# Kernel tuning notes

Hardware: AMD Instinct MI355X
Metric: run time of the kernel (lower is better)

## Reference

```python
import jax, jax.numpy as jnp
import numpy as np

TOP_K = 2


def setup_inputs() -> dict:
    key = jax.random.key(0)
    k_x, k_g, k_w1, k_w2, k_w3 = jax.random.split(key, 5)
    B, S, D, H, E = 2, 512, 1024, 512, 8
    x = jax.random.normal(k_x, (B, S, D), dtype=jnp.float32)
    gate_w = jax.random.normal(k_g, (D, E), dtype=jnp.float32) * (D ** -0.5)
    w1 = jax.random.normal(k_w1, (E, D, H), dtype=jnp.float32) * 0.02  # gate proj
    w2 = jax.random.normal(k_w2, (E, H, D), dtype=jnp.float32) * 0.02  # down proj
    w3 = jax.random.normal(k_w3, (E, D, H), dtype=jnp.float32) * 0.02  # up proj
    return {"x": x, "gate_w": gate_w, "w1": w1, "w2": w2, "w3": w3}


def reference(x, gate_w, w1, w2, w3):
    # Token-choice top-k MoE with grouped SwiGLU experts, no shared expert.
    # Equivalent to torchtune MoE: gather routed tokens, scale by top-k router
    # score, run per-expert FFN, scatter-add back. Since each expert's FFN has
    # no bias (FFN(0) == 0), the dispatch/grouped-GEMM/combine is expressed
    # densely as sum_e FFN_e(scale[:, e] * x), which is mathematically identical.
    B, S, D = x.shape
    E = gate_w.shape[1]
    xf = x.reshape(B * S, D)                      # [T, D]
    T = B * S

    logits = xf @ gate_w                          # [T, E]
    scores = jax.nn.softmax(logits, axis=-1)
    top_scores, top_idx = jax.lax.top_k(scores, TOP_K)  # [T, k]

    # scale[t, e] = router score if expert e selected for token t, else 0
    scale = jnp.zeros((T, E), dtype=x.dtype).at[
        jnp.arange(T)[:, None], top_idx
    ].set(top_scores)

    xs = scale.T[:, :, None] * xf[None, :, :]     # [E, T, D] scaled routed input
    h = jax.nn.silu(jnp.einsum('etd,edh->eth', xs, w1)) \
        * jnp.einsum('etd,edh->eth', xs, w3)      # [E, T, H]
    y = jnp.einsum('eth,ehd->etd', h, w2)         # [E, T, D]
    out = y.sum(axis=0)                           # combine (scatter-add equiv)
    return out.reshape(B, S, D)
```

## Files before the change

kernel.cpp:

```cpp
#include <hip/hip_runtime.h>
#include <hip/hip_bf16.h>
#include <cstddef>

#define T_TOK 1024
#define D_DIM 1024
#define H_DIM 512
#define E_EXP 8
#define P_CAP 2560
#define MAX_MT 72
#define LDA 72
#define NK1 16
#define NK2 8

typedef __attribute__((ext_vector_type(4))) float    float4_t;
typedef __attribute__((ext_vector_type(8))) short    short8_t;
typedef __attribute__((ext_vector_type(4))) unsigned uint4_t;
typedef __attribute__((ext_vector_type(2))) unsigned uint2_t;

__device__ __forceinline__ short f2bf(float f) {
  union { float f; unsigned u; } v; v.f = f;
  unsigned u = v.u;
  u += 0x7FFFu + ((u >> 16) & 1u);
  return (short)(u >> 16);
}

__device__ __forceinline__ unsigned pkbf(float a, float b) {
  union { __hip_bfloat162 h; unsigned u; } v;
  v.h = __float22bfloat162_rn(make_float2(a, b));
  return v.u;
}

__global__ __launch_bounds__(256) void prep_kernel(
    const float* __restrict__ w1, const float* __restrict__ w3,
    const float* __restrict__ w2, const float* __restrict__ x,
    const float* __restrict__ gw, short* __restrict__ w13t,
    short* __restrict__ w2t, int* __restrict__ idx2,
    float* __restrict__ scale2, float* __restrict__ out) {
  __shared__ float tile[64][69];
  const int z = blockIdx.z;
  const int tid = threadIdx.x;

  if (z < 24) {
    const float* src; short* dst; int N, ldd, row_off;
    if (z < 16) {
      if (blockIdx.y >= 8) return;
      int which = z >> 3, e = z & 7;
      src = (which ? w3 : w1) + (size_t)e * D_DIM * H_DIM;
      dst = w13t + (size_t)e * D_DIM * (2 * H_DIM);
      N = H_DIM; ldd = D_DIM; row_off = which ? H_DIM : 0;
    } else {
      if (blockIdx.x >= 8) return;
      int e = z - 16;
      src = w2 + (size_t)e * H_DIM * D_DIM;
      dst = w2t + (size_t)e * D_DIM * H_DIM;
      N = D_DIM; ldd = H_DIM; row_off = 0;
    }
    const int k0 = blockIdx.x * 64, n0 = blockIdx.y * 64;
    const int kr = tid >> 4, nc = (tid & 15) * 4;
    #pragma unroll
    for (int p = 0; p < 4; ++p) {
      int k = p * 16 + kr;
      float4_t v = *(const float4_t*)(src + (size_t)(k0 + k) * N + n0 + nc);
      tile[k][nc]     = v[0];
      tile[k][nc + 1] = v[1];
      tile[k][nc + 2] = v[2];
      tile[k][nc + 3] = v[3];
    }
    __syncthreads();
    const int r8 = tid >> 3, c8 = tid & 7;
    #pragma unroll
    for (int p = 0; p < 2; ++p) {
      int row = p * 32 + r8;
      uint4_t u;
      #pragma unroll
      for (int jj = 0; jj < 4; ++jj)
        u[jj] = pkbf(tile[c8 * 8 + 2 * jj][row], tile[c8 * 8 + 2 * jj + 1][row]);
      *(uint4_t*)(dst + (size_t)(row_off + n0 + row) * ldd + k0 + c8 * 8) = u;
    }
    return;
  }

  if (z == 25) {
    float4_t z4 = {0.f, 0.f, 0.f, 0.f};
    float4_t* o = (float4_t*)(out + ((size_t)(blockIdx.y * 16 + blockIdx.x)) * 4096);
    #pragma unroll
    for (int i = 0; i < 4; ++i) o[i * 256 + tid] = z4;
    return;
  }

  const int wid  = tid >> 6;
  const int lane = tid & 63;
  const int t = (blockIdx.y * 16 + blockIdx.x) * 4 + wid;
  const float* xr = x + (size_t)t * D_DIM;
  float acc[E_EXP];
  #pragma unroll
  for (int e = 0; e < E_EXP; ++e) acc[e] = 0.f;
  for (int d = lane; d < D_DIM; d += 64) {
    float xv = xr[d];
    float4_t g0 = *(const float4_t*)(gw + d * E_EXP);
    float4_t g1 = *(const float4_t*)(gw + d * E_EXP + 4);
    acc[0] += xv * g0[0]; acc[1] += xv * g0[1];
    acc[2] += xv * g0[2]; acc[3] += xv * g0[3];
    acc[4] += xv * g1[0]; acc[5] += xv * g1[1];
    acc[6] += xv * g1[2]; acc[7] += xv * g1[3];
  }
  #pragma unroll
  for (int off = 32; off >= 1; off >>= 1) {
    #pragma unroll
    for (int e = 0; e < E_EXP; ++e) acc[e] += __shfl_down(acc[e], off, 64);
  }
  if (lane == 0) {
    float m = acc[0];
    #pragma unroll
    for (int e = 1; e < E_EXP; ++e) m = fmaxf(m, acc[e]);
    float p[E_EXP]; float s = 0.f;
    #pragma unroll
    for (int e = 0; e < E_EXP; ++e) { p[e] = __expf(acc[e] - m); s += p[e]; }
    float inv = 1.f / s;
    #pragma unroll
    for (int e = 0; e < E_EXP; ++e) p[e] *= inv;
    int i1 = 0;
    #pragma unroll
    for (int e = 1; e < E_EXP; ++e) if (p[e] > p[i1]) i1 = e;
    int i2 = (i1 == 0) ? 1 : 0;
    #pragma unroll
    for (int e = 0; e < E_EXP; ++e) {
      if (e == i1 || e == i2) continue;
      if (p[e] > p[i2]) i2 = e;
    }
    idx2[2 * t]     = i1;  scale2[2 * t]     = p[i1];
    idx2[2 * t + 1] = i2;  scale2[2 * t + 1] = p[i2];
  }
}

__global__ __launch_bounds__(256) void scan_kernel(
    const int* __restrict__ idx2, const float* __restrict__ scale2,
    int* __restrict__ pair_tok, float* __restrict__ pair_scale,
    int* __restrict__ meta) {
  __shared__ int cnt[E_EXP], base[E_EXP], cur[E_EXP];
  const int tid = threadIdx.x;
  if (tid < E_EXP) { cnt[tid] = 0; cur[tid] = 0; }
  for (int p = tid; p < P_CAP; p += 256) { pair_tok[p] = -1; pair_scale[p] = 0.f; }
  __syncthreads();
  for (int t = tid; t < T_TOK; t += 256) {
    atomicAdd(&cnt[idx2[2 * t]], 1);
    atomicAdd(&cnt[idx2[2 * t + 1]], 1);
  }
  __syncthreads();
  if (tid == 0) {
    int b = 0, g = 0;
    for (int e = 0; e < E_EXP; ++e) {
      base[e] = b;
      int al = (cnt[e] + 31) & ~31;
      for (int j = 0; j < al; j += 32) { meta[1 + g] = e; meta[81 + g] = b + j; ++g; }
      b += al;
    }
    meta[0] = g;
  }
  __syncthreads();
  for (int t = tid; t < T_TOK; t += 256) {
    #pragma unroll
    for (int s = 0; s < 2; ++s) {
      int e = idx2[2 * t + s];
      int p = base[e] + atomicAdd(&cur[e], 1);
      pair_tok[p] = t;
      pair_scale[p] = scale2[2 * t + s];
    }
  }
}

__global__ __launch_bounds__(256) void astage_kernel(
    const float* __restrict__ x, const int* __restrict__ pair_tok,
    const float* __restrict__ pair_scale, short* __restrict__ Ag) {
  const int tid = threadIdx.x;
  const int row = blockIdx.x * 8 + (tid >> 5);
  const int c0  = (tid & 31) * 4;
  const int   tok = pair_tok[row];
  const float sc  = pair_scale[row];
  const float* xr = x + (size_t)(tok < 0 ? 0 : tok) * D_DIM;
  short* orow = Ag + (size_t)row * D_DIM;
  #pragma unroll
  for (int j = 0; j < 8; ++j) {
    int c = c0 + j * 128;
    float4_t v = *(const float4_t*)(xr + c);
    uint2_t u = { pkbf(v[0] * sc, v[1] * sc), pkbf(v[2] * sc, v[3] * sc) };
    *(uint2_t*)(orow + c) = u;
  }
}

__global__ __launch_bounds__(256, 5) void gemm1_kernel(
    const short* __restrict__ Ag, const short* __restrict__ w13t,
    const int* __restrict__ meta, short* __restrict__ h) {
  __shared__ short As[2][32 * LDA];
  __shared__ short B1s[2][32 * LDA];
  __shared__ short B3s[2][32 * LDA];
  const int mt = blockIdx.y;
  if (mt >= meta[0]) return;
  const int e    = meta[1 + mt];
  const int row0 = meta[81 + mt];
  const int n0   = blockIdx.x * 32;
  const int tid = threadIdx.x, lane = tid & 63, wid = tid >> 6;
  const int wr = wid >> 1, wc = wid & 1;
  const int q = lane >> 4, ln = lane & 15;
  const short* bsrc = w13t + (size_t)e * D_DIM * (2 * H_DIM);

  const int sr = tid >> 3, sk = (tid & 7) * 8;
  const short* ap  = Ag   + (size_t)(row0 + sr) * D_DIM + sk;
  const short* b1p = bsrc + (size_t)(n0 + sr) * D_DIM + sk;
  const short* b3p = bsrc + (size_t)(H_DIM + n0 + sr) * D_DIM + sk;

  float4_t acc1 = {0.f, 0.f, 0.f, 0.f}, acc3 = {0.f, 0.f, 0.f, 0.f};

  {
    uint4_t va = *(const uint4_t*)ap;
    uint4_t v1 = *(const uint4_t*)b1p;
    uint4_t v3 = *(const uint4_t*)b3p;
    *(uint4_t*)&As[0][sr * LDA + sk]  = va;
    *(uint4_t*)&B1s[0][sr * LDA + sk] = v1;
    *(uint4_t*)&B3s[0][sr * LDA + sk] = v3;
  }

  for (int t = 0; t < NK1 - 1; ++t) {
    __syncthreads();
    const int cur = t & 1, nxt = cur ^ 1;
    const int ko = (t + 1) * 64;
    uint4_t wa  = *(const uint4_t*)(ap + ko);
    uint4_t w1v = *(const uint4_t*)(b1p + ko);
    uint4_t w3v = *(const uint4_t*)(b3p + ko);

    short8_t af[2], b1f[2], b3f[2];
    #pragma unroll
    for (int kk = 0; kk < 2; ++kk) {
      af[kk]  = *(const short8_t*)&As[cur][(wr * 16 + ln) * LDA + kk * 32 + q * 8];
      b1f[kk] = *(const short8_t*)&B1s[cur][(wc * 16 + ln) * LDA + kk * 32 + q * 8];
      b3f[kk] = *(const short8_t*)&B3s[cur][(wc * 16 + ln) * LDA + kk * 32 + q * 8];
    }
    #pragma unroll
    for (int kk = 0; kk < 2; ++kk) {
      acc1 = __builtin_amdgcn_mfma_f32_16x16x32_bf16(af[kk], b1f[kk], acc1, 0, 0, 0);
      acc3 = __builtin_amdgcn_mfma_f32_16x16x32_bf16(af[kk], b3f[kk], acc3, 0, 0, 0);
    }
    *(uint4_t*)&As[nxt][sr * LDA + sk]  = wa;
    *(uint4_t*)&B1s[nxt][sr * LDA + sk] = w1v;
    *(uint4_t*)&B3s[nxt][sr * LDA + sk] = w3v;
  }
  __syncthreads();
  {
    short8_t af[2], b1f[2], b3f[2];
    #pragma unroll
    for (int kk = 0; kk < 2; ++kk) {
      af[kk]  = *(const short8_t*)&As[1][(wr * 16 + ln) * LDA + kk * 32 + q * 8];
      b1f[kk] = *(const short8_t*)&B1s[1][(wc * 16 + ln) * LDA + kk * 32 + q * 8];
      b3f[kk] = *(const short8_t*)&B3s[1][(wc * 16 + ln) * LDA + kk * 32 + q * 8];
    }
    #pragma unroll
    for (int kk = 0; kk < 2; ++kk) {
      acc1 = __builtin_amdgcn_mfma_f32_16x16x32_bf16(af[kk], b1f[kk], acc1, 0, 0, 0);
      acc3 = __builtin_amdgcn_mfma_f32_16x16x32_bf16(af[kk], b3f[kk], acc3, 0, 0, 0);
    }
  }

  {
    int r_base = row0 + wr * 16 + q * 4;
    int col = n0 + wc * 16 + ln;
    #pragma unroll
    for (int rr = 0; rr < 4; ++rr) {
      float c1 = acc1[rr];
      float c3 = acc3[rr];
      float sig = 1.f / (1.f + __expf(-c1));
      h[(size_t)(r_base + rr) * H_DIM + col] = f2bf(c1 * sig * c3);
    }
  }
}

__global__ __launch_bounds__(256, 5) void gemm2_kernel(
    const short* __restrict__ h, const short* __restrict__ w2t,
    const int* __restrict__ pair_tok, const int* __restrict__ meta,
    float* __restrict__ out) {
  __shared__ short As[2][32 * LDA];
  __shared__ short Bs[2][64 * LDA];
  const int mt = blockIdx.y;
  if (mt >= meta[0]) return;
  const int e    = meta[1 + mt];
  const int row0 = meta[81 + mt];
  const int n0   = blockIdx.x * 64;
  const int tid = threadIdx.x, lane = tid & 63, wid = tid >> 6;
  const int wr = wid >> 1, wc = wid & 1;
  const int q = lane >> 4, ln = lane & 15;
  const short* bsrc = w2t + (size_t)e * D_DIM * H_DIM;

  const int ar = tid >> 3, ak = (tid & 7) * 8;
  const short* arow = h + (size_t)(row0 + ar) * H_DIM + ak;
  const int br = tid >> 2, bk = (tid & 3) * 16;
  const short* brow = bsrc + (size_t)(n0 + br) * H_DIM + bk;

  float4_t acc[2];
  acc[0] = acc[1] = (float4_t){0.f, 0.f, 0.f, 0.f};

  {
    uint4_t va  = *(const uint4_t*)arow;
    uint4_t vb0 = *(const uint4_t*)brow;
    uint4_t vb1 = *(const uint4_t*)(brow + 8);
    *(uint4_t*)&As[0][ar * LDA + ak]     = va;
    *(uint4_t*)&Bs[0][br * LDA + bk]     = vb0;
    *(uint4_t*)&Bs[0][br * LDA + bk + 8] = vb1;
  }

  for (int t = 0; t < NK2 - 1; ++t) {
    __syncthreads();
    const int cur = t & 1, nxt = cur ^ 1;
    const int ko = (t + 1) * 64;
    uint4_t wa  = *(const uint4_t*)(arow + ko);
    uint4_t wb0 = *(const uint4_t*)(brow + ko);
    uint4_t wb1 = *(const uint4_t*)(brow + ko + 8);

    short8_t af[2], bf[2][2];
    #pragma unroll
    for (int kk = 0; kk < 2; ++kk) {
      af[kk] = *(const short8_t*)&As[cur][(wr * 16 + ln) * LDA + kk * 32 + q * 8];
      #pragma unroll
      for (int j = 0; j < 2; ++j)
        bf[j][kk] = *(const short8_t*)&Bs[cur][(wc * 32 + j * 16 + ln) * LDA + kk * 32 + q * 8];
    }
    #pragma unroll
    for (int j = 0; j < 2; ++j)
      #pragma unroll
      for (int kk = 0; kk < 2; ++kk)
        acc[j] = __builtin_amdgcn_mfma_f32_16x16x32_bf16(af[kk], bf[j][kk], acc[j], 0, 0, 0);

    *(uint4_t*)&As[nxt][ar * LDA + ak]     = wa;
    *(uint4_t*)&Bs[nxt][br * LDA + bk]     = wb0;
    *(uint4_t*)&Bs[nxt][br * LDA + bk + 8] = wb1;
  }
  __syncthreads();
  {
    short8_t af[2], bf[2][2];
    #pragma unroll
    for (int kk = 0; kk < 2; ++kk) {
      af[kk] = *(const short8_t*)&As[1][(wr * 16 + ln) * LDA + kk * 32 + q * 8];
      #pragma unroll
      for (int j = 0; j < 2; ++j)
        bf[j][kk] = *(const short8_t*)&Bs[1][(wc * 32 + j * 16 + ln) * LDA + kk * 32 + q * 8];
    }
    #pragma unroll
    for (int j = 0; j < 2; ++j)
      #pragma unroll
      for (int kk = 0; kk < 2; ++kk)
        acc[j] = __builtin_amdgcn_mfma_f32_16x16x32_bf16(af[kk], bf[j][kk], acc[j], 0, 0, 0);
  }

  {
    int r_base = row0 + wr * 16 + q * 4;
    #pragma unroll
    for (int rr = 0; rr < 4; ++rr) {
      int tok = pair_tok[r_base + rr];
      if (tok < 0) continue;
      float* orow = out + (size_t)tok * D_DIM;
      #pragma unroll
      for (int j = 0; j < 2; ++j) {
        int col = n0 + wc * 32 + j * 16 + ln;
        atomicAdd(orow + col, acc[j][rr]);
      }
    }
  }
}

extern "C" void kernel_launch(void* const* d_in, const int* in_sizes, int n_in,
                              void* d_out, int out_size, void* d_ws, size_t ws_size,
                              hipStream_t stream) {
  const float* x  = (const float*)d_in[0];
  const float* gw = (const float*)d_in[1];
  const float* w1 = (const float*)d_in[2];
  const float* w2 = (const float*)d_in[3];
  const float* w3 = (const float*)d_in[4];
  float* out = (float*)d_out;

  char* ws = (char*)d_ws;
  int*   idx2    = (int*)  (ws);
  float* scale2  = (float*)(ws + 8192);
  int*   ptok    = (int*)  (ws + 16384);
  float* pscale  = (float*)(ws + 32768);
  int*   meta    = (int*)  (ws + 49152);
  short* h       = (short*)(ws + (1u << 20));
  short* w13t    = (short*)(ws + (4u << 20));
  short* w2t     = (short*)(ws + (21u << 20));
  short* Ag      = (short*)(ws + (30u << 20));

  prep_kernel<<<dim3(16, 16, 26), dim3(256), 0, stream>>>(
      w1, w3, w2, x, gw, w13t, w2t, idx2, scale2, out);
  scan_kernel<<<dim3(1), dim3(256), 0, stream>>>(idx2, scale2, ptok, pscale, meta);
  astage_kernel<<<dim3(P_CAP / 8), dim3(256), 0, stream>>>(x, ptok, pscale, Ag);
  gemm1_kernel<<<dim3(H_DIM / 32, MAX_MT), dim3(256), 0, stream>>>(
      Ag, w13t, meta, h);
  gemm2_kernel<<<dim3(D_DIM / 64, MAX_MT), dim3(256), 0, stream>>>(
      h, w2t, ptok, meta, out);
}
```

Measured before the change: 147.3 us.

## Enlarge grouped-GEMM tiles to 64-row blocks using 32x32x16 MFMA

Both expert GEMMs now work on 64-row tiles (expert groups padded to multiples of 64) with wider N tiles, and use the 32x32x16 bf16 MFMA instead of 16x16x32. Each block reuses more of its loaded A and B data, and far fewer blocks read the weights. In exchange there is more padding waste per expert, fewer blocks in flight (launch bounds lowered to 2), and more registers per thread.

```diff
diff --git a/kernel.cpp b/kernel.cpp
--- a/kernel.cpp
+++ b/kernel.cpp
@@ -7,15 +7,16 @@
 #define H_DIM 512
 #define E_EXP 8
 #define P_CAP 2560
-#define MAX_MT 72
+#define MAX_MT 40
 #define LDA 72
 #define NK1 16
 #define NK2 8
 
-typedef __attribute__((ext_vector_type(4))) float    float4_t;
-typedef __attribute__((ext_vector_type(8))) short    short8_t;
-typedef __attribute__((ext_vector_type(4))) unsigned uint4_t;
-typedef __attribute__((ext_vector_type(2))) unsigned uint2_t;
+typedef __attribute__((ext_vector_type(4)))  float    float4_t;
+typedef __attribute__((ext_vector_type(16))) float    f32x16;
+typedef __attribute__((ext_vector_type(8)))  short    short8_t;
+typedef __attribute__((ext_vector_type(4)))  unsigned uint4_t;
+typedef __attribute__((ext_vector_type(2)))  unsigned uint2_t;
 
 __device__ __forceinline__ short f2bf(float f) {
   union { float f; unsigned u; } v; v.f = f;
@@ -151,8 +152,8 @@
     int b = 0, g = 0;
     for (int e = 0; e < E_EXP; ++e) {
       base[e] = b;
-      int al = (cnt[e] + 31) & ~31;
-      for (int j = 0; j < al; j += 32) { meta[1 + g] = e; meta[81 + g] = b + j; ++g; }
+      int al = (cnt[e] + 63) & ~63;
+      for (int j = 0; j < al; j += 64) { meta[1 + g] = e; meta[81 + g] = b + j; ++g; }
       b += al;
     }
     meta[0] = g;
@@ -188,178 +189,210 @@
   }
 }
 
-__global__ __launch_bounds__(256, 5) void gemm1_kernel(
+__global__ __launch_bounds__(256, 2) void gemm1_kernel(
     const short* __restrict__ Ag, const short* __restrict__ w13t,
     const int* __restrict__ meta, short* __restrict__ h) {
-  __shared__ short As[2][32 * LDA];
-  __shared__ short B1s[2][32 * LDA];
-  __shared__ short B3s[2][32 * LDA];
-  const int mt = blockIdx.y;
-  if (mt >= meta[0]) return;
-  const int e    = meta[1 + mt];
-  const int row0 = meta[81 + mt];
-  const int n0   = blockIdx.x * 32;
-  const int tid = threadIdx.x, lane = tid & 63, wid = tid >> 6;
-  const int wr = wid >> 1, wc = wid & 1;
-  const int q = lane >> 4, ln = lane & 15;
-  const short* bsrc = w13t + (size_t)e * D_DIM * (2 * H_DIM);
-
-  const int sr = tid >> 3, sk = (tid & 7) * 8;
-  const short* ap  = Ag   + (size_t)(row0 + sr) * D_DIM + sk;
-  const short* b1p = bsrc + (size_t)(n0 + sr) * D_DIM + sk;
-  const short* b3p = bsrc + (size_t)(H_DIM + n0 + sr) * D_DIM + sk;
-
-  float4_t acc1 = {0.f, 0.f, 0.f, 0.f}, acc3 = {0.f, 0.f, 0.f, 0.f};
-
-  {
-    uint4_t va = *(const uint4_t*)ap;
-    uint4_t v1 = *(const uint4_t*)b1p;
-    uint4_t v3 = *(const uint4_t*)b3p;
-    *(uint4_t*)&As[0][sr * LDA + sk]  = va;
-    *(uint4_t*)&B1s[0][sr * LDA + sk] = v1;
-    *(uint4_t*)&B3s[0][sr * LDA + sk] = v3;
-  }
-
-  for (int t = 0; t < NK1 - 1; ++t) {
-    __syncthreads();
-    const int cur = t & 1, nxt = cur ^ 1;
-    const int ko = (t + 1) * 64;
-    uint4_t wa  = *(const uint4_t*)(ap + ko);
-    uint4_t w1v = *(const uint4_t*)(b1p + ko);
-    uint4_t w3v = *(const uint4_t*)(b3p + ko);
-
-    short8_t af[2], b1f[2], b3f[2];
-    #pragma unroll
-    for (int kk = 0; kk < 2; ++kk) {
-      af[kk]  = *(const short8_t*)&As[cur][(wr * 16 + ln) * LDA + kk * 32 + q * 8];
-      b1f[kk] = *(const short8_t*)&B1s[cur][(wc * 16 + ln) * LDA + kk * 32 + q * 8];
-      b3f[kk] = *(const short8_t*)&B3s[cur][(wc * 16 + ln) * LDA + kk * 32 + q * 8];
-    }
-    #pragma unroll
-    for (int kk = 0; kk < 2; ++kk) {
-      acc1 = __builtin_amdgcn_mfma_f32_16x16x32_bf16(af[kk], b1f[kk], acc1, 0, 0, 0);
-      acc3 = __builtin_amdgcn_mfma_f32_16x16x32_bf16(af[kk], b3f[kk], acc3, 0, 0, 0);
-    }
-    *(uint4_t*)&As[nxt][sr * LDA + sk]  = wa;
-    *(uint4_t*)&B1s[nxt][sr * LDA + sk] = w1v;
-    *(uint4_t*)&B3s[nxt][sr * LDA + sk] = w3v;
-  }
-  __syncthreads();
-  {
-    short8_t af[2], b1f[2], b3f[2];
-    #pragma unroll
-    for (int kk = 0; kk < 2; ++kk) {
-      af[kk]  = *(const short8_t*)&As[1][(wr * 16 + ln) * LDA + kk * 32 + q * 8];
-      b1f[kk] = *(const short8_t*)&B1s[1][(wc * 16 + ln) * LDA + kk * 32 + q * 8];
-      b3f[kk] = *(const short8_t*)&B3s[1][(wc * 16 + ln) * LDA + kk * 32 + q * 8];
-    }
-    #pragma unroll
-    for (int kk = 0; kk < 2; ++kk) {
-      acc1 = __builtin_amdgcn_mfma_f32_16x16x32_bf16(af[kk], b1f[kk], acc1, 0, 0, 0);
-      acc3 = __builtin_amdgcn_mfma_f32_16x16x32_bf16(af[kk], b3f[kk], acc3, 0, 0, 0);
-    }
-  }
-
-  {
-    int r_base = row0 + wr * 16 + q * 4;
-    int col = n0 + wc * 16 + ln;
-    #pragma unroll
-    for (int rr = 0; rr < 4; ++rr) {
-      float c1 = acc1[rr];
-      float c3 = acc3[rr];
-      float sig = 1.f / (1.f + __expf(-c1));
-      h[(size_t)(r_base + rr) * H_DIM + col] = f2bf(c1 * sig * c3);
-    }
-  }
-}
-
-__global__ __launch_bounds__(256, 5) void gemm2_kernel(
-    const short* __restrict__ h, const short* __restrict__ w2t,
-    const int* __restrict__ pair_tok, const int* __restrict__ meta,
-    float* __restrict__ out) {
-  __shared__ short As[2][32 * LDA];
-  __shared__ short Bs[2][64 * LDA];
+  __shared__ short As[2][64 * LDA];
+  __shared__ short B1s[2][64 * LDA];
+  __shared__ short B3s[2][64 * LDA];
   const int mt = blockIdx.y;
   if (mt >= meta[0]) return;
   const int e    = meta[1 + mt];
   const int row0 = meta[81 + mt];
   const int n0   = blockIdx.x * 64;
   const int tid = threadIdx.x, lane = tid & 63, wid = tid >> 6;
-  const int wr = wid >> 1, wc = wid & 1;
-  const int q = lane >> 4, ln = lane & 15;
+  const int wm = wid >> 1, wn = wid & 1;
+  const int l31 = lane & 31, lh = lane >> 5;
+  const short* bsrc = w13t + (size_t)e * D_DIM * (2 * H_DIM);
+
+  const int sr = tid >> 3, su = (tid & 7) * 8;
+  const size_t st32 = (size_t)32 * D_DIM;
+  const short* apA = Ag   + (size_t)(row0 + sr) * D_DIM + su;
+  const short* ap1 = bsrc + (size_t)(n0 + sr) * D_DIM + su;
+  const short* ap3 = bsrc + (size_t)(H_DIM + n0 + sr) * D_DIM + su;
+
+  f32x16 acc1, acc3;
+  #pragma unroll
+  for (int i = 0; i < 16; ++i) { acc1[i] = 0.f; acc3[i] = 0.f; }
+
+  {
+    uint4_t a0 = *(const uint4_t*)apA;
+    uint4_t a1 = *(const uint4_t*)(apA + st32);
+    uint4_t p0 = *(const uint4_t*)ap1;
+    uint4_t p1 = *(const uint4_t*)(ap1 + st32);
+    uint4_t q0 = *(const uint4_t*)ap3;
+    uint4_t q1 = *(const uint4_t*)(ap3 + st32);
+    *(uint4_t*)&As[0][sr * LDA + su]         = a0;
+    *(uint4_t*)&As[0][(sr + 32) * LDA + su]  = a1;
+    *(uint4_t*)&B1s[0][sr * LDA + su]        = p0;
+    *(uint4_t*)&B1s[0][(sr + 32) * LDA + su] = p1;
+    *(uint4_t*)&B3s[0][sr * LDA + su]        = q0;
+    *(uint4_t*)&B3s[0][(sr + 32) * LDA + su] = q1;
+  }
+
+  for (int t = 0; t < NK1 - 1; ++t) {
+    __syncthreads();
+    const int cur = t & 1, nxt = cur ^ 1;
+    const int ko = (t + 1) * 64;
+    uint4_t a0 = *(const uint4_t*)(apA + ko);
+    uint4_t a1 = *(const uint4_t*)(apA + st32 + ko);
+    uint4_t p0 = *(const uint4_t*)(ap1 + ko);
+    uint4_t p1 = *(const uint4_t*)(ap1 + st32 + ko);
+    uint4_t q0 = *(const uint4_t*)(ap3 + ko);
+    uint4_t q1 = *(const uint4_t*)(ap3 + st32 + ko);
+
+    short8_t af[4], b1f[4], b3f[4];
+    #pragma unroll
+    for (int s = 0; s < 4; ++s) {
+      const int kof = s * 16 + lh * 8;
+      af[s]  = *(const short8_t*)&As[cur][(wm * 32 + l31) * LDA + kof];
+      b1f[s] = *(const short8_t*)&B1s[cur][(wn * 32 + l31) * LDA + kof];
+      b3f[s] = *(const short8_t*)&B3s[cur][(wn * 32 + l31) * LDA + kof];
+    }
+    #pragma unroll
+    for (int s = 0; s < 4; ++s) {
+      acc1 = __builtin_amdgcn_mfma_f32_32x32x16_bf16(af[s], b1f[s], acc1, 0, 0, 0);
+      acc3 = __builtin_amdgcn_mfma_f32_32x32x16_bf16(af[s], b3f[s], acc3, 0, 0, 0);
+    }
+    *(uint4_t*)&As[nxt][sr * LDA + su]         = a0;
+    *(uint4_t*)&As[nxt][(sr + 32) * LDA + su]  = a1;
+    *(uint4_t*)&B1s[nxt][sr * LDA + su]        = p0;
+    *(uint4_t*)&B1s[nxt][(sr + 32) * LDA + su] = p1;
+    *(uint4_t*)&B3s[nxt][sr * LDA + su]        = q0;
+    *(uint4_t*)&B3s[nxt][(sr + 32) * LDA + su] = q1;
+  }
+  __syncthreads();
+  {
+    short8_t af[4], b1f[4], b3f[4];
+    #pragma unroll
+    for (int s = 0; s < 4; ++s) {
+      const int kof = s * 16 + lh * 8;
+      af[s]  = *(const short8_t*)&As[1][(wm * 32 + l31) * LDA + kof];
+      b1f[s] = *(const short8_t*)&B1s[1][(wn * 32 + l31) * LDA + kof];
+      b3f[s] = *(const short8_t*)&B3s[1][(wn * 32 + l31) * LDA + kof];
+    }
+    #pragma unroll
+    for (int s = 0; s < 4; ++s) {
+      acc1 = __builtin_amdgcn_mfma_f32_32x32x16_bf16(af[s], b1f[s], acc1, 0, 0, 0);
+      acc3 = __builtin_amdgcn_mfma_f32_32x32x16_bf16(af[s], b3f[s], acc3, 0, 0, 0);
+    }
+  }
+
+  {
+    const int col = n0 + wn * 32 + l31;
+    #pragma unroll
+    for (int r = 0; r < 16; ++r) {
+      int mrow = (r & 3) + 8 * (r >> 2) + 4 * lh;
+      int grow = row0 + wm * 32 + mrow;
+      float c1 = acc1[r], c3 = acc3[r];
+      float sig = 1.f / (1.f + __expf(-c1));
+      h[(size_t)grow * H_DIM + col] = f2bf(c1 * sig * c3);
+    }
+  }
+}
+
+__global__ __launch_bounds__(256, 2) void gemm2_kernel(
+    const short* __restrict__ h, const short* __restrict__ w2t,
+    const int* __restrict__ pair_tok, const int* __restrict__ meta,
+    float* __restrict__ out) {
+  __shared__ short As[2][64 * LDA];
+  __shared__ short Bs[2][128 * LDA];
+  const int mt = blockIdx.y;
+  if (mt >= meta[0]) return;
+  const int e    = meta[1 + mt];
+  const int row0 = meta[81 + mt];
+  const int n0   = blockIdx.x * 128;
+  const int tid = threadIdx.x, lane = tid & 63, wid = tid >> 6;
+  const int wm = wid >> 1, wn = wid & 1;
+  const int l31 = lane & 31, lh = lane >> 5;
   const short* bsrc = w2t + (size_t)e * D_DIM * H_DIM;
 
-  const int ar = tid >> 3, ak = (tid & 7) * 8;
-  const short* arow = h + (size_t)(row0 + ar) * H_DIM + ak;
-  const int br = tid >> 2, bk = (tid & 3) * 16;
-  const short* brow = bsrc + (size_t)(n0 + br) * H_DIM + bk;
-
-  float4_t acc[2];
-  acc[0] = acc[1] = (float4_t){0.f, 0.f, 0.f, 0.f};
-
-  {
-    uint4_t va  = *(const uint4_t*)arow;
-    uint4_t vb0 = *(const uint4_t*)brow;
-    uint4_t vb1 = *(const uint4_t*)(brow + 8);
-    *(uint4_t*)&As[0][ar * LDA + ak]     = va;
-    *(uint4_t*)&Bs[0][br * LDA + bk]     = vb0;
-    *(uint4_t*)&Bs[0][br * LDA + bk + 8] = vb1;
+  const int sr = tid >> 3, su = (tid & 7) * 8;
+  const size_t st32 = (size_t)32 * H_DIM;
+  const short* apA = h    + (size_t)(row0 + sr) * H_DIM + su;
+  const short* apB = bsrc + (size_t)(n0 + sr) * H_DIM + su;
+
+  f32x16 acc[2];
+  #pragma unroll
+  for (int i = 0; i < 16; ++i) { acc[0][i] = 0.f; acc[1][i] = 0.f; }
+
+  {
+    uint4_t a0 = *(const uint4_t*)apA;
+    uint4_t a1 = *(const uint4_t*)(apA + st32);
+    uint4_t b0 = *(const uint4_t*)apB;
+    uint4_t b1 = *(const uint4_t*)(apB + st32);
+    uint4_t b2 = *(const uint4_t*)(apB + 2 * st32);
+    uint4_t b3 = *(const uint4_t*)(apB + 3 * st32);
+    *(uint4_t*)&As[0][sr * LDA + su]         = a0;
+    *(uint4_t*)&As[0][(sr + 32) * LDA + su]  = a1;
+    *(uint4_t*)&Bs[0][sr * LDA + su]         = b0;
+    *(uint4_t*)&Bs[0][(sr + 32) * LDA + su]  = b1;
+    *(uint4_t*)&Bs[0][(sr + 64) * LDA + su]  = b2;
+    *(uint4_t*)&Bs[0][(sr + 96) * LDA + su]  = b3;
   }
 
   for (int t = 0; t < NK2 - 1; ++t) {
     __syncthreads();
     const int cur = t & 1, nxt = cur ^ 1;
     const int ko = (t + 1) * 64;
-    uint4_t wa  = *(const uint4_t*)(arow + ko);
-    uint4_t wb0 = *(const uint4_t*)(brow + ko);
-    uint4_t wb1 = *(const uint4_t*)(brow + ko + 8);
-
-    short8_t af[2], bf[2][2];
-    #pragma unroll
-    for (int kk = 0; kk < 2; ++kk) {
-      af[kk] = *(const short8_t*)&As[cur][(wr * 16 + ln) * LDA + kk * 32 + q * 8];
+    uint4_t a0 = *(const uint4_t*)(apA + ko);
+    uint4_t a1 = *(const uint4_t*)(apA + st32 + ko);
+    uint4_t b0 = *(const uint4_t*)(apB + ko);
+    uint4_t b1 = *(const uint4_t*)(apB + st32 + ko);
+    uint4_t b2 = *(const uint4_t*)(apB + 2 * st32 + ko);
+    uint4_t b3 = *(const uint4_t*)(apB + 3 * st32 + ko);
+
+    short8_t af[4], bf[2][4];
+    #pragma unroll
+    for (int s = 0; s < 4; ++s) {
+      const int kof = s * 16 + lh * 8;
+      af[s] = *(const short8_t*)&As[cur][(wm * 32 + l31) * LDA + kof];
       #pragma unroll
       for (int j = 0; j < 2; ++j)
-        bf[j][kk] = *(const short8_t*)&Bs[cur][(wc * 32 + j * 16 + ln) * LDA + kk * 32 + q * 8];
-    }
-    #pragma unroll
-    for (int j = 0; j < 2; ++j)
-      #pragma unroll
-      for (int kk = 0; kk < 2; ++kk)
-        acc[j] = __builtin_amdgcn_mfma_f32_16x16x32_bf16(af[kk], bf[j][kk], acc[j], 0, 0, 0);
-
-    *(uint4_t*)&As[nxt][ar * LDA + ak]     = wa;
-    *(uint4_t*)&Bs[nxt][br * LDA + bk]     = wb0;
-    *(uint4_t*)&Bs[nxt][br * LDA + bk + 8] = wb1;
+        bf[j][s] = *(const short8_t*)&Bs[cur][(wn * 64 + j * 32 + l31) * LDA + kof];
+    }
+    #pragma unroll
+    for (int s = 0; s < 4; ++s) {
+      acc[0] = __builtin_amdgcn_mfma_f32_32x32x16_bf16(af[s], bf[0][s], acc[0], 0, 0, 0);
+      acc[1] = __builtin_amdgcn_mfma_f32_32x32x16_bf16(af[s], bf[1][s], acc[1], 0, 0, 0);
+    }
+    *(uint4_t*)&As[nxt][sr * LDA + su]         = a0;
+    *(uint4_t*)&As[nxt][(sr + 32) * LDA + su]  = a1;
+    *(uint4_t*)&Bs[nxt][sr * LDA + su]         = b0;
+    *(uint4_t*)&Bs[nxt][(sr + 32) * LDA + su]  = b1;
+    *(uint4_t*)&Bs[nxt][(sr + 64) * LDA + su]  = b2;
+    *(uint4_t*)&Bs[nxt][(sr + 96) * LDA + su]  = b3;
   }
   __syncthreads();
   {
-    short8_t af[2], bf[2][2];
-    #pragma unroll
-    for (int kk = 0; kk < 2; ++kk) {
-      af[kk] = *(const short8_t*)&As[1][(wr * 16 + ln) * LDA + kk * 32 + q * 8];
+    short8_t af[4], bf[2][4];
+    #pragma unroll
+    for (int s = 0; s < 4; ++s) {
+      const int kof = s * 16 + lh * 8;
+      af[s] = *(const short8_t*)&As[1][(wm * 32 + l31) * LDA + kof];
       #pragma unroll
       for (int j = 0; j < 2; ++j)
-        bf[j][kk] = *(const short8_t*)&Bs[1][(wc * 32 + j * 16 + ln) * LDA + kk * 32 + q * 8];
-    }
-    #pragma unroll
-    for (int j = 0; j < 2; ++j)
-      #pragma unroll
-      for (int kk = 0; kk < 2; ++kk)
-        acc[j] = __builtin_amdgcn_mfma_f32_16x16x32_bf16(af[kk], bf[j][kk], acc[j], 0, 0, 0);
-  }
-
-  {
-    int r_base = row0 + wr * 16 + q * 4;
-    #pragma unroll
-    for (int rr = 0; rr < 4; ++rr) {
-      int tok = pair_tok[r_base + rr];
+        bf[j][s] = *(const short8_t*)&Bs[1][(wn * 64 + j * 32 + l31) * LDA + kof];
+    }
+    #pragma unroll
+    for (int s = 0; s < 4; ++s) {
+      acc[0] = __builtin_amdgcn_mfma_f32_32x32x16_bf16(af[s], bf[0][s], acc[0], 0, 0, 0);
+      acc[1] = __builtin_amdgcn_mfma_f32_32x32x16_bf16(af[s], bf[1][s], acc[1], 0, 0, 0);
+    }
+  }
+
+  {
+    #pragma unroll
+    for (int r = 0; r < 16; ++r) {
+      int mrow = (r & 3) + 8 * (r >> 2) + 4 * lh;
+      int grow = row0 + wm * 32 + mrow;
+      int tok = pair_tok[grow];
       if (tok < 0) continue;
       float* orow = out + (size_t)tok * D_DIM;
       #pragma unroll
       for (int j = 0; j < 2; ++j) {
-        int col = n0 + wc * 32 + j * 16 + ln;
-        atomicAdd(orow + col, acc[j][rr]);
+        int col = n0 + wn * 64 + j * 32 + l31;
+        atomicAdd(orow + col, acc[j][r]);
       }
     }
   }
@@ -390,8 +423,8 @@
       w1, w3, w2, x, gw, w13t, w2t, idx2, scale2, out);
   scan_kernel<<<dim3(1), dim3(256), 0, stream>>>(idx2, scale2, ptok, pscale, meta);
   astage_kernel<<<dim3(P_CAP / 8), dim3(256), 0, stream>>>(x, ptok, pscale, Ag);
-  gemm1_kernel<<<dim3(H_DIM / 32, MAX_MT), dim3(256), 0, stream>>>(
+  gemm1_kernel<<<dim3(H_DIM / 64, MAX_MT), dim3(256), 0, stream>>>(
       Ag, w13t, meta, h);
-  gemm2_kernel<<<dim3(D_DIM / 64, MAX_MT), dim3(256), 0, stream>>>(
+  gemm2_kernel<<<dim3(D_DIM / 128, MAX_MT), dim3(256), 0, stream>>>(
       h, w2t, ptok, meta, out);
 }
```

Measured after the change: 148.5 us. Within noise of the previous version (+0.8%).
